# Kernel tuning notes

Hardware: AMD Instinct MI355X
Metric: run time of the kernel (lower is better)

## Reference

```python
import jax, jax.numpy as jnp
import numpy as np

# Module hyperparameters (from init_kwargs)
K = 1.0                       # init_curvature (registered buffer, non-trainable)
HOPFIELD_DIM = 64
BETA = 1.0 / np.sqrt(float(HOPFIELD_DIM))  # beta=None default -> 1/sqrt(d_h)
EPS = 1e-7

# ---- Lorentz / hyperboloid ops (geoopt conventions, curvature param k>0) ----

def _to_tangent0(x):
    # x: (..., d) Euclidean -> (..., d+1) in T_0 H via [0, x], norm-clipped to 3.5
    zeros = jnp.zeros(x.shape[:-1] + (1,), x.dtype)
    x = jnp.concatenate([zeros, x], axis=-1)
    n = jnp.linalg.norm(x, axis=-1, keepdims=True)
    factor = jnp.minimum(3.5 / (n + 1e-7), 1.0)
    return x * factor

def expmap0(x_euc):
    # (..., d) Euclidean -> (..., d+1) on hyperboloid via Exp_0([0, x])
    u = _to_tangent0(x_euc)
    x = u[..., 1:]
    sqrtk = jnp.sqrt(K)
    xn = jnp.maximum(jnp.linalg.norm(x, axis=-1, keepdims=True), EPS)
    theta = xn / sqrtk
    return jnp.concatenate(
        [sqrtk * jnp.cosh(theta), sqrtk * jnp.sinh(theta) * x / xn], axis=-1)

def logmap0(y):
    # (..., d+1) on hyperboloid -> (..., d) tangent at origin (spatial part)
    sqrtk = jnp.sqrt(K)
    y0 = y[..., :1]
    yr = y[..., 1:]
    yn = jnp.maximum(jnp.linalg.norm(yr, axis=-1, keepdims=True), EPS)
    d = sqrtk * jnp.arccosh(jnp.maximum(y0 / sqrtk, 1.0 + EPS))
    return d * yr / yn

def minkowski_inner(u, v):
    # <u,v>_L = -u0 v0 + sum_i u_i v_i ; returns (...) without last dim
    return -u[..., 0] * v[..., 0] + jnp.sum(u[..., 1:] * v[..., 1:], axis=-1)

# ---- KFCore forward ----

def _kfcore(queries, keys, values, Wq, bq, Wk, bk, Wv, bv):
    sqrtk = jnp.sqrt(K)
    Qe = queries @ Wq.T + bq                     # (B,S,d_h)
    Ke = keys @ Wk.T + bk                        # (B,M,d_h)
    Ve = (values @ Wk.T + bk) @ Wv.T + bv        # (B,M,d_out)
    Q = expmap0(Qe)                              # (B,S,d+1)
    Kh = expmap0(Ke)                             # (B,M,d+1)
    V = expmap0(Ve)                              # (B,M,d+1)

    dp1 = Q.shape[-1]
    sign = jnp.concatenate([-jnp.ones((1,), Q.dtype), jnp.ones((dp1 - 1,), Q.dtype)])

    # Minkowski inner pairwise: (B,S,M)
    sims = jnp.einsum('bsd,bmd->bsm', Q * sign, Kh)
    alpha = jax.nn.softmax(-BETA * sims, axis=-1)          # (B,S,M)

    # Karcher flow: tangent_mean = sum_m alpha * logmap_Q(V_m)
    # logmap_x(y) = dist(x,y) * (y + (<x,y>/k) x) / ||y + (<x,y>/k) x||_L
    ip = jnp.einsum('bsd,bmd->bsm', Q * sign, V)           # <Q_s, V_m>_L
    dist = sqrtk * jnp.arccosh(jnp.maximum(-ip / K, 1.0 + EPS))
    qq = minkowski_inner(Q, Q)[:, :, None]                 # (B,S,1)
    vv = minkowski_inner(V, V)[:, None, :]                 # (B,1,M)
    c = ip / K
    nomin_sq = vv + 2.0 * c * ip + c * c * qq              # ||nomin||_L^2, (B,S,M)
    denom = jnp.sqrt(jnp.maximum(nomin_sq, EPS))
    w = alpha * dist / denom                               # (B,S,M)
    # sum_m w * (V_m + c * Q_s)  -- avoids the (B,S,M,d+1) logmap tensor
    tm = jnp.einsum('bsm,bmd->bsd', w, V) \
         + jnp.sum(w * c, axis=-1, keepdims=True) * Q      # (B,S,d+1)

    # expmap_Q(tm) = cosh(||tm||/sqrtk) Q + sqrtk sinh(||tm||/sqrtk) tm/||tm||
    un = jnp.sqrt(jnp.maximum(minkowski_inner(tm, tm), EPS))[..., None]
    th = un / sqrtk
    z = jnp.cosh(th) * Q + sqrtk * jnp.sinh(th) * tm / un
    return logmap0(z)                                      # (B,S,d_out)


def setup_inputs() -> dict:
    key = jax.random.key(0)
    ks = jax.random.split(key, 9)
    B, S, M = 2, 2048, 4096
    SD, MD, DH, DO = 256, 256, 64, 64
    sq = 1.0 / np.sqrt(SD)
    sm = 1.0 / np.sqrt(MD)
    sh = 1.0 / np.sqrt(DH)
    return {
        'queries': jax.random.normal(ks[0], (B, S, SD), jnp.float32),
        'keys':    jax.random.normal(ks[1], (B, M, MD), jnp.float32),
        'values':  jax.random.normal(ks[2], (B, M, MD), jnp.float32),
        'Wq': jax.random.normal(ks[3], (DH, SD), jnp.float32) * sq,
        'bq': jax.random.normal(ks[4], (DH,), jnp.float32) * sq,
        'Wk': jax.random.normal(ks[5], (DH, MD), jnp.float32) * sm,
        'bk': jax.random.normal(ks[6], (DH,), jnp.float32) * sm,
        'Wv': jax.random.normal(ks[7], (DO, DH), jnp.float32) * sh,
        'bv': jax.random.normal(ks[8], (DO,), jnp.float32) * sh,
    }


def reference(queries, keys, values, Wq, bq, Wk, bk, Wv, bv):
    return _kfcore(queries, keys, values, Wq, bq, Wk, bk, Wv, bv)
```

## Files before the change

### kernel.cpp

```cpp
#include <hip/hip_runtime.h>
#include <math.h>

#define BETA  0.125f
#define SHIFT 30.0f
#define EPSF  1e-7f

typedef __attribute__((ext_vector_type(8))) short short8;
typedef __attribute__((ext_vector_type(4))) short short4v;
typedef __attribute__((ext_vector_type(4))) float f32x4;

__device__ __forceinline__ unsigned short bf16_rne(float x) {
  unsigned int u = __float_as_uint(x);
  return (unsigned short)((u + 0x7fffu + ((u >> 16) & 1u)) >> 16);
}
__device__ __forceinline__ float bf16_tof(unsigned short h) {
  return __uint_as_float(((unsigned int)h) << 16);
}
__device__ __forceinline__ void split2(float x, unsigned short& h, unsigned short& l) {
  unsigned int u = __float_as_uint(x);
  unsigned int hr = (u + 0x7fffu + ((u >> 16) & 1u)) & 0xffff0000u;
  h = (unsigned short)(hr >> 16);
  l = bf16_rne(x - __uint_as_float(hr));
}
__device__ __forceinline__ void split8(float4 a, float4 b, short8& h8, short8& l8) {
  unsigned short h, l;
  split2(a.x, h, l); h8[0] = (short)h; l8[0] = (short)l;
  split2(a.y, h, l); h8[1] = (short)h; l8[1] = (short)l;
  split2(a.z, h, l); h8[2] = (short)h; l8[2] = (short)l;
  split2(a.w, h, l); h8[3] = (short)h; l8[3] = (short)l;
  split2(b.x, h, l); h8[4] = (short)h; l8[4] = (short)l;
  split2(b.y, h, l); h8[5] = (short)h; l8[5] = (short)l;
  split2(b.z, h, l); h8[6] = (short)h; l8[6] = (short)l;
  split2(b.w, h, l); h8[7] = (short)h; l8[7] = (short)l;
}

#define ZERO_F4 68608

__global__ __launch_bounds__(256) void proj_kernel(
    const float* __restrict__ Xq, const float* __restrict__ Xk,
    const float* __restrict__ Xv,
    const float* __restrict__ Wq, const float* __restrict__ bq,
    const float* __restrict__ Wk, const float* __restrict__ bk,
    const float* __restrict__ Wv, const float* __restrict__ bv,
    float* __restrict__ Q0, float* __restrict__ K0, float* __restrict__ V0,
    unsigned short* __restrict__ Qh, unsigned short* __restrict__ Ql,
    unsigned short* __restrict__ Kh, unsigned short* __restrict__ Kl,
    unsigned short* __restrict__ Vh, unsigned short* __restrict__ Vl,
    unsigned short* __restrict__ Vth, unsigned short* __restrict__ Vtl,
    float* __restrict__ zeroRegion)
{
  __shared__ unsigned int Tr[64 * 65];
  __shared__ unsigned short VkL[4][2][16 * 72];

  const int bid = blockIdx.x;
  const int tid = threadIdx.x;

  {
    int idx = bid * 256 + tid;
    if (idx < ZERO_F4)
      *(float4*)&zeroRegion[idx * 4] = make_float4(0.f, 0.f, 0.f, 0.f);
  }

  const float *X, *W, *bias;
  float* y0;
  unsigned short *yh, *yl;
  bool dbl;
  int rowBase;
  if (bid < 128)      { X = Xv; W = Wk; bias = bk; y0 = V0; yh = Vh; yl = Vl; rowBase = bid << 6;         dbl = true;  }
  else if (bid < 256) { X = Xk; W = Wk; bias = bk; y0 = K0; yh = Kh; yl = Kl; rowBase = (bid - 128) << 6; dbl = false; }
  else                { X = Xq; W = Wq; bias = bq; y0 = Q0; yh = Qh; yl = Ql; rowBase = (bid - 256) << 6; dbl = false; }

  const int wave = tid >> 6, lane = tid & 63;
  const int lm = lane & 15;
  const int lg = lane >> 4;
  const int rowB = rowBase + (wave << 4);

  short8 Ah[8], Al[8];
  {
    const float* Xr = X + (rowB + lm) * 256 + lg * 8;
#pragma unroll
    for (int ks = 0; ks < 8; ++ks) {
      float4 x0 = *(const float4*)&Xr[ks * 32];
      float4 x1 = *(const float4*)&Xr[ks * 32 + 4];
      split8(x0, x1, Ah[ks], Al[ks]);
    }
  }

  f32x4 acc[4];
#pragma unroll
  for (int nj = 0; nj < 4; ++nj) {
    float b = bias[nj * 16 + lm];
    acc[nj] = f32x4{b, b, b, b};
  }
#pragma unroll
  for (int nj = 0; nj < 4; ++nj) {
    const float* Wr = W + (nj * 16 + lm) * 256 + lg * 8;
#pragma unroll
    for (int ks = 0; ks < 8; ++ks) {
      float4 w0 = *(const float4*)&Wr[ks * 32];
      float4 w1 = *(const float4*)&Wr[ks * 32 + 4];
      short8 Bh, Bl;
      split8(w0, w1, Bh, Bl);
      acc[nj] = __builtin_amdgcn_mfma_f32_16x16x32_bf16(Ah[ks], Bh, acc[nj], 0, 0, 0);
      acc[nj] = __builtin_amdgcn_mfma_f32_16x16x32_bf16(Ah[ks], Bl, acc[nj], 0, 0, 0);
      acc[nj] = __builtin_amdgcn_mfma_f32_16x16x32_bf16(Al[ks], Bh, acc[nj], 0, 0, 0);
    }
  }

  if (dbl) {
    unsigned short* vh_ = &VkL[wave][0][0];
    unsigned short* vl_ = &VkL[wave][1][0];
#pragma unroll
    for (int nj = 0; nj < 4; ++nj)
#pragma unroll
      for (int r = 0; r < 4; ++r) {
        unsigned short h, l;
        split2(acc[nj][r], h, l);
        vh_[(lg * 4 + r) * 72 + nj * 16 + lm] = h;
        vl_[(lg * 4 + r) * 72 + nj * 16 + lm] = l;
      }
    __syncthreads();
    short8 A2h[2], A2l[2];
#pragma unroll
    for (int ks = 0; ks < 2; ++ks) {
      A2h[ks] = *(const short8*)&vh_[lm * 72 + ks * 32 + lg * 8];
      A2l[ks] = *(const short8*)&vl_[lm * 72 + ks * 32 + lg * 8];
    }
#pragma unroll
    for (int nj = 0; nj < 4; ++nj) {
      float b = bv[nj * 16 + lm];
      acc[nj] = f32x4{b, b, b, b};
    }
#pragma unroll
    for (int nj = 0; nj < 4; ++nj) {
      const float* Wr = Wv + (nj * 16 + lm) * 64 + lg * 8;
#pragma unroll
      for (int ks = 0; ks < 2; ++ks) {
        float4 w0 = *(const float4*)&Wr[ks * 32];
        float4 w1 = *(const float4*)&Wr[ks * 32 + 4];
        short8 Bh, Bl;
        split8(w0, w1, Bh, Bl);
        acc[nj] = __builtin_amdgcn_mfma_f32_16x16x32_bf16(A2h[ks], Bh, acc[nj], 0, 0, 0);
        acc[nj] = __builtin_amdgcn_mfma_f32_16x16x32_bf16(A2h[ks], Bl, acc[nj], 0, 0, 0);
        acc[nj] = __builtin_amdgcn_mfma_f32_16x16x32_bf16(A2l[ks], Bh, acc[nj], 0, 0, 0);
      }
    }
  }

  float n2p[4];
#pragma unroll
  for (int r = 0; r < 4; ++r)
    n2p[r] = acc[0][r] * acc[0][r] + acc[1][r] * acc[1][r] +
             acc[2][r] * acc[2][r] + acc[3][r] * acc[3][r];
#pragma unroll
  for (int r = 0; r < 4; ++r) {
    n2p[r] += __shfl_xor(n2p[r], 1);
    n2p[r] += __shfl_xor(n2p[r], 2);
    n2p[r] += __shfl_xor(n2p[r], 4);
    n2p[r] += __shfl_xor(n2p[r], 8);
  }
  unsigned short hv[4][4], lv[4][4];
#pragma unroll
  for (int r = 0; r < 4; ++r) {
    float n = sqrtf(n2p[r]);
    float factor = fminf(3.5f / (n + EPSF), 1.0f);
    float xn = fmaxf(n * factor, EPSF);
    float et = __expf(xn);
    float rt = __builtin_amdgcn_rcpf(et);
    float ch = 0.5f * (et + rt);
    float sh = 0.5f * (et - rt);
    float scale = sh * factor * __builtin_amdgcn_rcpf(xn);
    int row = rowB + lg * 4 + r;
    if (lm == 0) y0[row] = ch;
#pragma unroll
    for (int nj = 0; nj < 4; ++nj) {
      split2(acc[nj][r] * scale, hv[r][nj], lv[r][nj]);
      yh[row * 64 + nj * 16 + lm] = hv[r][nj];
      yl[row * 64 + nj * 16 + lm] = lv[r][nj];
    }
  }

  if (dbl) {
#pragma unroll
    for (int r = 0; r < 4; ++r)
#pragma unroll
      for (int nj = 0; nj < 4; ++nj)
        Tr[(wave * 16 + lg * 4 + r) * 65 + nj * 16 + lm] = (unsigned int)hv[r][nj];
    __syncthreads();
#pragma unroll
    for (int q = 0; q < 2; ++q) {
      int f = tid + (q << 8);
      int d = f >> 3;
      int seg = (f & 7) << 3;
      unsigned int o[4];
#pragma unroll
      for (int k = 0; k < 4; ++k)
        o[k] = Tr[(seg + 2 * k) * 65 + d] | (Tr[(seg + 2 * k + 1) * 65 + d] << 16);
      *(uint4*)&Vth[d * 8192 + rowBase + seg] = make_uint4(o[0], o[1], o[2], o[3]);
    }
    __syncthreads();
#pragma unroll
    for (int r = 0; r < 4; ++r)
#pragma unroll
      for (int nj = 0; nj < 4; ++nj)
        Tr[(wave * 16 + lg * 4 + r) * 65 + nj * 16 + lm] = (unsigned int)lv[r][nj];
    __syncthreads();
#pragma unroll
    for (int q = 0; q < 2; ++q) {
      int f = tid + (q << 8);
      int d = f >> 3;
      int seg = (f & 7) << 3;
      unsigned int o[4];
#pragma unroll
      for (int k = 0; k < 4; ++k)
        o[k] = Tr[(seg + 2 * k) * 65 + d] | (Tr[(seg + 2 * k + 1) * 65 + d] << 16);
      *(uint4*)&Vtl[d * 8192 + rowBase + seg] = make_uint4(o[0], o[1], o[2], o[3]);
    }
  }
}

__global__ void __attribute__((amdgpu_waves_per_eu(4)))
__launch_bounds__(256) attn_kernel(
    const float* __restrict__ Q0g, const unsigned short* __restrict__ Qh,
    const unsigned short* __restrict__ Ql,
    const float* __restrict__ K0g, const unsigned short* __restrict__ Khg,
    const unsigned short* __restrict__ Klg,
    const float* __restrict__ V0g, const unsigned short* __restrict__ Vhg,
    const unsigned short* __restrict__ Vlg,
    const unsigned short* __restrict__ Vthg, const unsigned short* __restrict__ Vtlg,
    float* __restrict__ Tacc, float* __restrict__ T0acc,
    float* __restrict__ Lacc, float* __restrict__ WCacc)
{
  __shared__ unsigned short LB[16640];

  const int tid = threadIdx.x;
  const int wave = tid >> 6, lane = tid & 63;
  const int lm = lane & 15;
  const int lg = lane >> 4;
  const int bid = blockIdx.x;
  const int slice = bid & 15;
  const int t = bid >> 4;
  const int b = t >> 5;
  const int sT = t & 31;
  const int sBase = b * 2048 + sT * 64 + wave * 16;

  unsigned short* wbase = LB + 14336 + wave * 576;

  short8 qf[2][2];
#pragma unroll
  for (int ks = 0; ks < 2; ++ks) {
    int idx = (sBase + lm) * 64 + ks * 32 + lg * 8;
    qf[ks][0] = *(const short8*)(Qh + idx);
    qf[ks][1] = *(const short8*)(Ql + idx);
  }
  float q0r[4];
#pragma unroll
  for (int r = 0; r < 4; ++r) q0r[r] = Q0g[sBase + lg * 4 + r];

  f32x4 accT[4];
  float Lp[4], WCp[4], T0p[4];
#pragma unroll
  for (int r = 0; r < 4; ++r) { Lp[r] = 0.f; WCp[r] = 0.f; T0p[r] = 0.f; }
#pragma unroll
  for (int dj = 0; dj < 4; ++dj) accT[dj] = f32x4{0.f, 0.f, 0.f, 0.f};

  const int mSliceBase = b * 4096 + slice * 256;
  const int srow = tid >> 3;
  const int sc8 = (tid & 7) << 3;
  const int drow = tid >> 2;
  const int dseg = (tid & 3) << 3;

  for (int mc = 0; mc < 8; ++mc) {
    const int mCh = mSliceBase + (mc << 5);

    {
      int goff = (mCh + srow) * 64 + sc8;
      int loff = srow * 72 + sc8;
      *(uint4*)&LB[loff]         = *(const uint4*)&Khg[goff];
      *(uint4*)&LB[2304 + loff]  = *(const uint4*)&Klg[goff];
      *(uint4*)&LB[4608 + loff]  = *(const uint4*)&Vhg[goff];
      *(uint4*)&LB[6912 + loff]  = *(const uint4*)&Vlg[goff];
      int gofft = drow * 8192 + mCh + dseg;
      int lofft = drow * 40 + dseg;
      *(uint4*)&LB[9216 + lofft]  = *(const uint4*)&Vthg[gofft];
      *(uint4*)&LB[11776 + lofft] = *(const uint4*)&Vtlg[gofft];
    }
    float k0r[2], v0r[2];
#pragma unroll
    for (int mj = 0; mj < 2; ++mj) {
      k0r[mj] = K0g[mCh + mj * 16 + lm];
      v0r[mj] = V0g[mCh + mj * 16 + lm];
    }
    __syncthreads();

#pragma unroll
    for (int mj = 0; mj < 2; ++mj) {
      f32x4 sims = f32x4{0.f, 0.f, 0.f, 0.f};
      f32x4 ipv  = f32x4{0.f, 0.f, 0.f, 0.f};
#pragma unroll
      for (int ks = 0; ks < 2; ++ks) {
        int off = (mj * 16 + lm) * 72 + ks * 32 + lg * 8;
        short8 kh = *(const short8*)&LB[off];
        short8 kl = *(const short8*)&LB[2304 + off];
        short8 vh = *(const short8*)&LB[4608 + off];
        short8 vl = *(const short8*)&LB[6912 + off];
        sims = __builtin_amdgcn_mfma_f32_16x16x32_bf16(qf[ks][0], kh, sims, 0, 0, 0);
        sims = __builtin_amdgcn_mfma_f32_16x16x32_bf16(qf[ks][0], kl, sims, 0, 0, 0);
        sims = __builtin_amdgcn_mfma_f32_16x16x32_bf16(qf[ks][1], kh, sims, 0, 0, 0);
        ipv  = __builtin_amdgcn_mfma_f32_16x16x32_bf16(qf[ks][0], vh, ipv, 0, 0, 0);
        ipv  = __builtin_amdgcn_mfma_f32_16x16x32_bf16(qf[ks][0], vl, ipv, 0, 0, 0);
        ipv  = __builtin_amdgcn_mfma_f32_16x16x32_bf16(qf[ks][1], vh, ipv, 0, 0, 0);
      }
#pragma unroll
      for (int r = 0; r < 4; ++r) {
        float c  = ipv[r]  - q0r[r] * v0r[mj];
        float sm = sims[r] - q0r[r] * k0r[mj];
        float x = -c;
        float s2 = fmaxf(fmaf(x, x, -1.0f), EPSF);
        float rs = __builtin_amdgcn_rsqf(s2);
        float dist = __logf(fmaf(s2, rs, x));
        float e = __expf(fmaf(-BETA, sm, -SHIFT));
        float w = e * dist * rs;
        unsigned short wu = bf16_rne(w);
        float wb = bf16_tof(wu);
        Lp[r]  += e;
        WCp[r] += wb * c;
        T0p[r] += wb * v0r[mj];
        wbase[(lg * 4 + r) * 36 + mj * 16 + lm] = wu;
      }
    }

    {
      short8 wa;
      {
        const unsigned short* p = wbase + lm * 36 + lg * 8;
        short4v a0 = *(const short4v*)p;
        short4v a1 = *(const short4v*)(p + 4);
        wa = __builtin_shufflevector(a0, a1, 0, 1, 2, 3, 4, 5, 6, 7);
      }
#pragma unroll
      for (int dj = 0; dj < 4; ++dj) {
        int off = (dj * 16 + lm) * 40 + lg * 8;
        short8 th = *(const short8*)&LB[9216 + off];
        short8 tl = *(const short8*)&LB[11776 + off];
        accT[dj] = __builtin_amdgcn_mfma_f32_16x16x32_bf16(wa, th, accT[dj], 0, 0, 0);
        accT[dj] = __builtin_amdgcn_mfma_f32_16x16x32_bf16(wa, tl, accT[dj], 0, 0, 0);
      }
    }
    __syncthreads();
  }

#pragma unroll
  for (int r = 0; r < 4; ++r)
#pragma unroll
    for (int off = 1; off < 16; off <<= 1) {
      Lp[r]  += __shfl_xor(Lp[r], off);
      WCp[r] += __shfl_xor(WCp[r], off);
      T0p[r] += __shfl_xor(T0p[r], off);
    }

#pragma unroll
  for (int r = 0; r < 4; ++r) {
    int row = sBase + lg * 4 + r;
#pragma unroll
    for (int dj = 0; dj < 4; ++dj)
      unsafeAtomicAdd(&Tacc[row * 64 + dj * 16 + lm], accT[dj][r]);
    if (lm == 0) {
      unsafeAtomicAdd(&Lacc[row],  Lp[r]);
      unsafeAtomicAdd(&WCacc[row], WCp[r]);
      unsafeAtomicAdd(&T0acc[row], T0p[r]);
    }
  }
}

__global__ __launch_bounds__(256) void combine_kernel(
    const float* __restrict__ Q0, const unsigned short* __restrict__ Qh,
    const unsigned short* __restrict__ Ql,
    const float* __restrict__ Tacc, const float* __restrict__ T0acc,
    const float* __restrict__ Lacc, const float* __restrict__ WCacc,
    float* __restrict__ out)
{
  int wid = (blockIdx.x << 2) + (threadIdx.x >> 6);
  int lane = threadIdx.x & 63;

  int qi = wid * 64 + lane;
  float Tsum = Tacc[qi];
  float T0 = T0acc[wid];
  float L  = Lacc[wid];
  float WC = WCacc[wid];

  float qd = bf16_tof(Qh[qi]) + bf16_tof(Ql[qi]);
  float q0 = Q0[wid];
  float invL = 1.0f / L;
  float td = Tsum * invL;
  float t0 = T0 * invL;
  float wc = WC * invL;

  double tt = (double)td * (double)td;
#pragma unroll
  for (int off = 1; off < 64; off <<= 1) tt += __shfl_xor(tt, off);
  tt -= (double)t0 * (double)t0;
  double mk = tt + (double)wc * (double)wc;

  float un = (float)sqrt(fmax(mk, 1e-12));
  float eu = __expf(un);
  float ru = 1.0f / eu;
  float ch = 0.5f * (eu + ru);
  float shu = 0.5f * (eu - ru) / un;

  float tmd = td + wc * qd;
  float tm0 = t0 + wc * q0;
  float zd = ch * qd + shu * tmd;
  float z0 = ch * q0 + shu * tm0;

  float p2 = zd * zd;
#pragma unroll
  for (int off = 1; off < 64; off <<= 1) p2 += __shfl_xor(p2, off);
  float yn = fmaxf(sqrtf(p2), EPSF);
  float zc = fmaxf(z0, 1.0f + EPSF);
  float dl = __logf(zc + sqrtf(fmaxf(zc * zc - 1.0f, 0.f)));
  out[qi] = dl * zd / yn;
}

extern "C" void kernel_launch(void* const* d_in, const int* in_sizes, int n_in,
                              void* d_out, int out_size, void* d_ws, size_t ws_size,
                              hipStream_t stream)
{
  const float* queries = (const float*)d_in[0];
  const float* keys    = (const float*)d_in[1];
  const float* values  = (const float*)d_in[2];
  const float* Wq      = (const float*)d_in[3];
  const float* bq      = (const float*)d_in[4];
  const float* Wk      = (const float*)d_in[5];
  const float* bk      = (const float*)d_in[6];
  const float* Wv      = (const float*)d_in[7];
  const float* bv      = (const float*)d_in[8];
  float* out = (float*)d_out;
  float* ws  = (float*)d_ws;

  float* Q0 = ws;
  float* K0 = ws + 4096;
  float* V0 = ws + 12288;
  unsigned short* Qh  = (unsigned short*)(ws + 20480);
  unsigned short* Ql  = (unsigned short*)(ws + 151552);
  unsigned short* Kh  = (unsigned short*)(ws + 282624);
  unsigned short* Kl  = (unsigned short*)(ws + 544768);
  unsigned short* Vh  = (unsigned short*)(ws + 806912);
  unsigned short* Vl  = (unsigned short*)(ws + 1069056);
  unsigned short* Vth = (unsigned short*)(ws + 1331200);
  unsigned short* Vtl = (unsigned short*)(ws + 1593344);
  float* Tacc  = ws + 1855488;
  float* T0acc = ws + 2117632;
  float* Lacc  = ws + 2121728;
  float* WCacc = ws + 2125824;

  proj_kernel<<<320, 256, 0, stream>>>(queries, keys, values, Wq, bq, Wk, bk,
                                       Wv, bv, Q0, K0, V0, Qh, Ql, Kh, Kl,
                                       Vh, Vl, Vth, Vtl, Tacc);
  attn_kernel<<<1024, 256, 0, stream>>>(
      Q0, Qh, Ql, K0, Kh, Kl, V0, Vh, Vl, Vth, Vtl,
      Tacc, T0acc, Lacc, WCacc);
  combine_kernel<<<1024, 256, 0, stream>>>(
      Q0, Qh, Ql, Tacc, T0acc, Lacc, WCacc, out);
}
```

Baseline: 144.6 us.

## Stage projection inputs and weights through shared memory in K-chunks

The projection kernel now loads the X tile and the weight matrix cooperatively into a single shared buffer in 64-wide K chunks, splitting each value into bf16 hi/lo once before the MFMA loop reads fragments from LDS. Before this, every wave loaded and split the whole weight matrix from global memory on its own, which repeated the split arithmetic and caused strided loads. The Wv weights for the second projection go through the same staging, and the transpose buffer reuses the same LDS space. This adds several block-wide barriers and LDS traffic per chunk, and it affects only the projection stage of the pipeline.

```diff
diff --git a/kernel.cpp b/kernel.cpp
--- a/kernel.cpp
+++ b/kernel.cpp
@@ -22,16 +22,14 @@
   h = (unsigned short)(hr >> 16);
   l = bf16_rne(x - __uint_as_float(hr));
 }
-__device__ __forceinline__ void split8(float4 a, float4 b, short8& h8, short8& l8) {
-  unsigned short h, l;
-  split2(a.x, h, l); h8[0] = (short)h; l8[0] = (short)l;
-  split2(a.y, h, l); h8[1] = (short)h; l8[1] = (short)l;
-  split2(a.z, h, l); h8[2] = (short)h; l8[2] = (short)l;
-  split2(a.w, h, l); h8[3] = (short)h; l8[3] = (short)l;
-  split2(b.x, h, l); h8[4] = (short)h; l8[4] = (short)l;
-  split2(b.y, h, l); h8[5] = (short)h; l8[5] = (short)l;
-  split2(b.z, h, l); h8[6] = (short)h; l8[6] = (short)l;
-  split2(b.w, h, l); h8[7] = (short)h; l8[7] = (short)l;
+__device__ __forceinline__ void store4(unsigned short* ph, unsigned short* pl, float4 v) {
+  unsigned short h0, h1, h2, h3, l0, l1, l2, l3;
+  split2(v.x, h0, l0); split2(v.y, h1, l1);
+  split2(v.z, h2, l2); split2(v.w, h3, l3);
+  *(uint2*)ph = make_uint2((unsigned)h0 | ((unsigned)h1 << 16),
+                           (unsigned)h2 | ((unsigned)h3 << 16));
+  *(uint2*)pl = make_uint2((unsigned)l0 | ((unsigned)l1 << 16),
+                           (unsigned)l2 | ((unsigned)l3 << 16));
 }
 
 #define ZERO_F4 68608
@@ -49,8 +47,7 @@
     unsigned short* __restrict__ Vth, unsigned short* __restrict__ Vtl,
     float* __restrict__ zeroRegion)
 {
-  __shared__ unsigned int Tr[64 * 65];
-  __shared__ unsigned short VkL[4][2][16 * 72];
+  __shared__ unsigned short LB[18432];
 
   const int bid = blockIdx.x;
   const int tid = threadIdx.x;
@@ -75,56 +72,73 @@
   const int lg = lane >> 4;
   const int rowB = rowBase + (wave << 4);
 
-  short8 Ah[8], Al[8];
-  {
-    const float* Xr = X + (rowB + lm) * 256 + lg * 8;
-#pragma unroll
-    for (int ks = 0; ks < 8; ++ks) {
-      float4 x0 = *(const float4*)&Xr[ks * 32];
-      float4 x1 = *(const float4*)&Xr[ks * 32 + 4];
-      split8(x0, x1, Ah[ks], Al[ks]);
-    }
-  }
-
   f32x4 acc[4];
 #pragma unroll
   for (int nj = 0; nj < 4; ++nj) {
     float b = bias[nj * 16 + lm];
     acc[nj] = f32x4{b, b, b, b};
   }
-#pragma unroll
-  for (int nj = 0; nj < 4; ++nj) {
-    const float* Wr = W + (nj * 16 + lm) * 256 + lg * 8;
-#pragma unroll
-    for (int ks = 0; ks < 8; ++ks) {
-      float4 w0 = *(const float4*)&Wr[ks * 32];
-      float4 w1 = *(const float4*)&Wr[ks * 32 + 4];
-      short8 Bh, Bl;
-      split8(w0, w1, Bh, Bl);
-      acc[nj] = __builtin_amdgcn_mfma_f32_16x16x32_bf16(Ah[ks], Bh, acc[nj], 0, 0, 0);
-      acc[nj] = __builtin_amdgcn_mfma_f32_16x16x32_bf16(Ah[ks], Bl, acc[nj], 0, 0, 0);
-      acc[nj] = __builtin_amdgcn_mfma_f32_16x16x32_bf16(Al[ks], Bh, acc[nj], 0, 0, 0);
-    }
+
+  for (int kc = 0; kc < 4; ++kc) {
+#pragma unroll
+    for (int q = 0; q < 4; ++q) {
+      int f = tid + (q << 8);
+      int r = f >> 4, g = f & 15;
+      float4 xv = *(const float4*)&X[(rowBase + r) * 256 + (kc << 6) + (g << 2)];
+      float4 wv = *(const float4*)&W[r * 256 + (kc << 6) + (g << 2)];
+      int o = r * 72 + (g << 2);
+      store4(&LB[o],         &LB[4608 + o],  xv);
+      store4(&LB[9216 + o],  &LB[13824 + o], wv);
+    }
+    __syncthreads();
+    short8 Ah2[2], Al2[2];
+#pragma unroll
+    for (int ks = 0; ks < 2; ++ks) {
+      int ao = (wave * 16 + lm) * 72 + ks * 32 + lg * 8;
+      Ah2[ks] = *(const short8*)&LB[ao];
+      Al2[ks] = *(const short8*)&LB[4608 + ao];
+    }
+#pragma unroll
+    for (int nj = 0; nj < 4; ++nj) {
+#pragma unroll
+      for (int ks = 0; ks < 2; ++ks) {
+        int bo = (nj * 16 + lm) * 72 + ks * 32 + lg * 8;
+        short8 Bh = *(const short8*)&LB[9216 + bo];
+        short8 Bl = *(const short8*)&LB[13824 + bo];
+        acc[nj] = __builtin_amdgcn_mfma_f32_16x16x32_bf16(Ah2[ks], Bh, acc[nj], 0, 0, 0);
+        acc[nj] = __builtin_amdgcn_mfma_f32_16x16x32_bf16(Ah2[ks], Bl, acc[nj], 0, 0, 0);
+        acc[nj] = __builtin_amdgcn_mfma_f32_16x16x32_bf16(Al2[ks], Bh, acc[nj], 0, 0, 0);
+      }
+    }
+    __syncthreads();
   }
 
   if (dbl) {
-    unsigned short* vh_ = &VkL[wave][0][0];
-    unsigned short* vl_ = &VkL[wave][1][0];
 #pragma unroll
     for (int nj = 0; nj < 4; ++nj)
 #pragma unroll
       for (int r = 0; r < 4; ++r) {
         unsigned short h, l;
         split2(acc[nj][r], h, l);
-        vh_[(lg * 4 + r) * 72 + nj * 16 + lm] = h;
-        vl_[(lg * 4 + r) * 72 + nj * 16 + lm] = l;
-      }
+        int ro = (wave * 16 + lg * 4 + r) * 72 + nj * 16 + lm;
+        LB[ro] = h;
+        LB[4608 + ro] = l;
+      }
+#pragma unroll
+    for (int q = 0; q < 4; ++q) {
+      int f = tid + (q << 8);
+      int r = f >> 4, g = f & 15;
+      float4 wv = *(const float4*)&Wv[r * 64 + (g << 2)];
+      int o = r * 72 + (g << 2);
+      store4(&LB[9216 + o], &LB[13824 + o], wv);
+    }
     __syncthreads();
     short8 A2h[2], A2l[2];
 #pragma unroll
     for (int ks = 0; ks < 2; ++ks) {
-      A2h[ks] = *(const short8*)&vh_[lm * 72 + ks * 32 + lg * 8];
-      A2l[ks] = *(const short8*)&vl_[lm * 72 + ks * 32 + lg * 8];
+      int ao = (wave * 16 + lm) * 72 + ks * 32 + lg * 8;
+      A2h[ks] = *(const short8*)&LB[ao];
+      A2l[ks] = *(const short8*)&LB[4608 + ao];
     }
 #pragma unroll
     for (int nj = 0; nj < 4; ++nj) {
@@ -133,13 +147,11 @@
     }
 #pragma unroll
     for (int nj = 0; nj < 4; ++nj) {
-      const float* Wr = Wv + (nj * 16 + lm) * 64 + lg * 8;
 #pragma unroll
       for (int ks = 0; ks < 2; ++ks) {
-        float4 w0 = *(const float4*)&Wr[ks * 32];
-        float4 w1 = *(const float4*)&Wr[ks * 32 + 4];
-        short8 Bh, Bl;
-        split8(w0, w1, Bh, Bl);
+        int bo = (nj * 16 + lm) * 72 + ks * 32 + lg * 8;
+        short8 Bh = *(const short8*)&LB[9216 + bo];
+        short8 Bl = *(const short8*)&LB[13824 + bo];
         acc[nj] = __builtin_amdgcn_mfma_f32_16x16x32_bf16(A2h[ks], Bh, acc[nj], 0, 0, 0);
         acc[nj] = __builtin_amdgcn_mfma_f32_16x16x32_bf16(A2h[ks], Bl, acc[nj], 0, 0, 0);
         acc[nj] = __builtin_amdgcn_mfma_f32_16x16x32_bf16(A2l[ks], Bh, acc[nj], 0, 0, 0);
@@ -181,6 +193,8 @@
   }
 
   if (dbl) {
+    __syncthreads();
+    unsigned int* Tr = (unsigned int*)LB;
 #pragma unroll
     for (int r = 0; r < 4; ++r)
 #pragma unroll
```

Result: faster. 135.2 us (-6.5%).
